# Kernel optimization log

Measured on AMD Instinct MI355X. Metric: run time of the kernel, lower is better.

Reference implementation:

```python
import jax, jax.numpy as jnp
import numpy as np

N, M, K = 100000, 50000, 8   # num vertices, num hyperedges, fixed hyperedge size
DIN, DOUT = 128, 128

def setup_inputs() -> dict:
    key = jax.random.key(0)
    k1, k2, k3 = jax.random.split(key, 3)
    X = jax.random.normal(k1, (N, DIN), jnp.float32)
    vertex = jax.random.randint(k2, (M * K,), 0, N)          # member vertices, flattened
    edges = jnp.repeat(jnp.arange(M), K)                     # hyperedge id per entry (sorted)
    W = jax.random.normal(k3, (DIN, DOUT), jnp.float32) / np.sqrt(DIN)
    b = jnp.zeros((DOUT,), jnp.float32)
    return {"X": X, "vertex": vertex, "edges": edges, "W": W, "b": b}

def reference(X, vertex, edges, W, b):
    # theta: Linear(in, out) applied BEFORE graph construction (as in dhg.HyperGCNConv)
    Y = X @ W + b                              # [N, DOUT]
    verts = vertex.reshape(M, K)               # hyperedge membership (edges = repeat(arange(M), K))
    feats = Y[verts]                           # [M, K, DOUT] gather
    # pairwise squared distances within each hyperedge
    sq = jnp.sum(feats * feats, axis=-1)                      # [M, K]
    d2 = sq[:, :, None] + sq[:, None, :] - 2.0 * jnp.einsum('mkd,mld->mkl', feats, feats)
    flat = jnp.argmax(d2.reshape(M, K * K), axis=1)
    ui, vi = flat // K, flat % K                              # argmax-distance pair positions
    u = jnp.take_along_axis(verts, ui[:, None], 1)[:, 0]      # [M]
    v = jnp.take_along_axis(verts, vi[:, None], 1)[:, 0]      # [M]
    w = jnp.float32(1.0 / (2 * K - 3))                        # HyperGCN mediator weight
    pos = jnp.arange(K)
    med = ((pos[None, :] != ui[:, None]) & (pos[None, :] != vi[:, None])).astype(Y.dtype)  # [M,K]
    # graph edges: (u,v) + (u,m),(v,m) for each mediator m; masked entries get weight 0
    src = jnp.concatenate([u, jnp.repeat(u, K), jnp.repeat(v, K)])
    dst = jnp.concatenate([v, verts.reshape(-1), verts.reshape(-1)])
    wts = jnp.concatenate([jnp.full((M,), w, Y.dtype), (med * w).reshape(-1), (med * w).reshape(-1)])
    # GCN smoothing: D^{-1/2} (A + I) D^{-1/2} Y with symmetric A, duplicate edges summed
    deg = jnp.ones((N,), Y.dtype).at[src].add(wts).at[dst].add(wts)
    dinv = jax.lax.rsqrt(deg)
    Xs = Y * dinv[:, None]
    out = Xs                                                  # self-loop term
    out = out.at[dst].add(wts[:, None] * Xs[src])
    out = out.at[src].add(wts[:, None] * Xs[dst])
    out = out * dinv[:, None]
    return jax.nn.relu(out)                                   # is_last=False -> ReLU (dropout=0)
```

## Files before the change

### kernel.cpp

```cpp
#include <hip/hip_runtime.h>
#include <hip/hip_bf16.h>

#define NV 100000
#define ME 50000
#define NINC (ME * 8)
#define NBLK ((NV + 255) / 256)
constexpr float WMED = 1.0f / 13.0f;

typedef __attribute__((ext_vector_type(8))) short bf16x8;
typedef __attribute__((ext_vector_type(4))) float f32x4;

static __device__ inline void cvt_split8(const float4& a, const float4& b,
                                         bf16x8& hi, bf16x8& lo) {
    const float v[8] = {a.x, a.y, a.z, a.w, b.x, b.y, b.z, b.w};
    #pragma unroll
    for (int j = 0; j < 8; ++j) {
        __hip_bfloat16 h = __float2bfloat16(v[j]);
        const float hf = __bfloat162float(h);
        __hip_bfloat16 l = __float2bfloat16(v[j] - hf);
        union { __hip_bfloat16 b; short s; } uh{h}, ul{l};
        hi[j] = uh.s;
        lo[j] = ul.s;
    }
}

__global__ __launch_bounds__(512, 4) void k_gemm(const float* __restrict__ X,
                                                 const float* __restrict__ W,
                                                 const float* __restrict__ bias,
                                                 float* __restrict__ Y,
                                                 __hip_bfloat16* __restrict__ Ybf) {
    __shared__ bf16x8 sWh[2048];
    __shared__ bf16x8 sWl[2048];
    const int t = threadIdx.x;
    const int wv = t >> 6;
    const int L  = t & 63;
    const int m  = L & 15;
    const int q  = L >> 4;

    for (int idx = t; idx < 128 * 32; idx += 512) {
        const int k  = idx >> 5;
        const int c4 = (idx & 31) * 4;
        const float4 w = *(const float4*)(W + (long)k * 128 + c4);
        const float wv4[4] = {w.x, w.y, w.z, w.w};
        short* swh = (short*)sWh;
        short* swl = (short*)sWl;
        const int s = k >> 5, qq = (k >> 3) & 3, j = k & 7;
        #pragma unroll
        for (int j2 = 0; j2 < 4; ++j2) {
            const int c = c4 + j2;
            const int frag = (s * 8 + (c >> 4)) * 64 + qq * 16 + (c & 15);
            __hip_bfloat16 h = __float2bfloat16(wv4[j2]);
            const float hf = __bfloat162float(h);
            __hip_bfloat16 l = __float2bfloat16(wv4[j2] - hf);
            union { __hip_bfloat16 b; short s; } uh{h}, ul{l};
            swh[frag * 8 + j] = uh.s;
            swl[frag * 8 + j] = ul.s;
        }
    }
    __syncthreads();

    f32x4 acc[2][8];
    #pragma unroll
    for (int tt = 0; tt < 2; ++tt)
        #pragma unroll
        for (int g = 0; g < 8; ++g)
            acc[tt][g] = (f32x4){0.f, 0.f, 0.f, 0.f};

    const int row_base = blockIdx.x * 256 + wv * 32;
    int r0 = row_base + m;      if (r0 > NV - 1) r0 = NV - 1;
    int r1 = row_base + 16 + m; if (r1 > NV - 1) r1 = NV - 1;

    #pragma unroll
    for (int s = 0; s < 4; ++s) {
        const int kb = s * 32 + q * 8;
        const float4 a00 = *(const float4*)(X + (long)r0 * 128 + kb);
        const float4 a01 = *(const float4*)(X + (long)r0 * 128 + kb + 4);
        const float4 a10 = *(const float4*)(X + (long)r1 * 128 + kb);
        const float4 a11 = *(const float4*)(X + (long)r1 * 128 + kb + 4);
        bf16x8 ah0, al0, ah1, al1;
        cvt_split8(a00, a01, ah0, al0);
        cvt_split8(a10, a11, ah1, al1);
        #pragma unroll
        for (int g = 0; g < 8; ++g) {
            const bf16x8 bh = sWh[(s * 8 + g) * 64 + L];
            const bf16x8 bl = sWl[(s * 8 + g) * 64 + L];
            acc[0][g] = __builtin_amdgcn_mfma_f32_16x16x32_bf16(ah0, bh, acc[0][g], 0, 0, 0);
            acc[0][g] = __builtin_amdgcn_mfma_f32_16x16x32_bf16(ah0, bl, acc[0][g], 0, 0, 0);
            acc[0][g] = __builtin_amdgcn_mfma_f32_16x16x32_bf16(al0, bh, acc[0][g], 0, 0, 0);
            acc[1][g] = __builtin_amdgcn_mfma_f32_16x16x32_bf16(ah1, bh, acc[1][g], 0, 0, 0);
            acc[1][g] = __builtin_amdgcn_mfma_f32_16x16x32_bf16(ah1, bl, acc[1][g], 0, 0, 0);
            acc[1][g] = __builtin_amdgcn_mfma_f32_16x16x32_bf16(al1, bh, acc[1][g], 0, 0, 0);
        }
    }

    #pragma unroll
    for (int g = 0; g < 8; ++g) {
        const int col = g * 16 + m;
        const float bc = bias[col];
        #pragma unroll
        for (int tt = 0; tt < 2; ++tt) {
            #pragma unroll
            for (int r = 0; r < 4; ++r) {
                const int row = row_base + tt * 16 + q * 4 + r;
                const float v = acc[tt][g][r] + bc;
                const float vn = __shfl_xor(v, 1);
                if (row < NV) {
                    Y[(long)row * 128 + col] = v;
                    if ((L & 1) == 0) {
                        __hip_bfloat162 h2;
                        h2.x = __float2bfloat16(v);
                        h2.y = __float2bfloat16(vn);
                        *(__hip_bfloat162*)(Ybf + (long)row * 128 + col) = h2;
                    }
                }
            }
        }
    }
}

__global__ __launch_bounds__(256) void k_edge(const float* __restrict__ Y,
                                              const int* __restrict__ vertex,
                                              int* __restrict__ uvpos) {
    __shared__ float sF[4][8 * 132];
    const int wid = threadIdx.x >> 6;
    const int lane = threadIdx.x & 63;
    const int m = blockIdx.x * 4 + wid;
    float* F = sF[wid];

    int verts[8];
    #pragma unroll
    for (int p = 0; p < 8; ++p) verts[p] = vertex[m * 8 + p];

    #pragma unroll
    for (int p = 0; p < 8; ++p) {
        const float2 v = *(const float2*)(Y + (long)verts[p] * 128 + lane * 2);
        *(float2*)(F + p * 132 + lane * 2) = v;
    }
    __syncthreads();

    const int k = lane >> 3, l = lane & 7;
    float acc = 0.0f;
    const float4* ra = (const float4*)(F + k * 132);
    const float4* rb = (const float4*)(F + l * 132);
    #pragma unroll
    for (int d4 = 0; d4 < 32; ++d4) {
        const float4 a = ra[d4], b = rb[d4];
        acc = fmaf(a.x, b.x, acc);
        acc = fmaf(a.y, b.y, acc);
        acc = fmaf(a.z, b.z, acc);
        acc = fmaf(a.w, b.w, acc);
    }
    const float sqk = __shfl(acc, k * 9);
    const float sql = __shfl(acc, l * 9);
    float v = sqk + sql - 2.0f * acc;
    int idx = lane;
    #pragma unroll
    for (int off = 32; off >= 1; off >>= 1) {
        const float ov = __shfl_xor(v, off);
        const int oi = __shfl_xor(idx, off);
        if (ov > v || (ov == v && oi < idx)) { v = ov; idx = oi; }
    }
    if (lane == 0) uvpos[m] = idx;
}

__global__ __launch_bounds__(256) void k_init(int* __restrict__ cnt,
                                              int* __restrict__ rowptr) {
    const int i = blockIdx.x * 256 + threadIdx.x;
    if (i < NV) cnt[i] = 0;
    if (i == 0) rowptr[NV] = NINC;
}

__global__ __launch_bounds__(256) void k_hist(const int* __restrict__ vertex,
                                              int* __restrict__ cnt) {
    const int j = blockIdx.x * 256 + threadIdx.x;
    if (j < NINC) atomicAdd(cnt + vertex[j], 1);
}

__global__ __launch_bounds__(256) void k_scan1(const int* __restrict__ cnt,
                                               int* __restrict__ bsum) {
    __shared__ int s[256];
    const int t = threadIdx.x;
    const int i = blockIdx.x * 256 + t;
    s[t] = (i < NV) ? cnt[i] : 0;
    __syncthreads();
    #pragma unroll
    for (int off = 128; off >= 1; off >>= 1) {
        if (t < off) s[t] += s[t + off];
        __syncthreads();
    }
    if (t == 0) bsum[blockIdx.x] = s[0];
}

__global__ __launch_bounds__(64) void k_scan2(const int* __restrict__ bsum,
                                              int* __restrict__ boff) {
    const int lane = threadIdx.x;
    int running = 0;
    for (int c = 0; c * 64 < NBLK; ++c) {
        const int idx = c * 64 + lane;
        int v = (idx < NBLK) ? bsum[idx] : 0;
        int x = v;
        #pragma unroll
        for (int off = 1; off < 64; off <<= 1) {
            const int n = __shfl_up(x, off);
            if (lane >= off) x += n;
        }
        if (idx < NBLK) boff[idx] = running + x - v;
        running += __shfl(x, 63);
    }
}

__global__ __launch_bounds__(256) void k_scan3(const int* __restrict__ cnt,
                                               const int* __restrict__ boff,
                                               int* __restrict__ rowptr,
                                               int* __restrict__ fill) {
    __shared__ int s[256];
    const int t = threadIdx.x;
    const int i = blockIdx.x * 256 + t;
    const int v = (i < NV) ? cnt[i] : 0;
    s[t] = v;
    __syncthreads();
    #pragma unroll
    for (int off = 1; off < 256; off <<= 1) {
        const int add = (t >= off) ? s[t - off] : 0;
        __syncthreads();
        s[t] += add;
        __syncthreads();
    }
    if (i < NV) {
        const int excl = boff[blockIdx.x] + s[t] - v;
        rowptr[i] = excl;
        fill[i] = excl;
    }
}

__global__ __launch_bounds__(256) void k_fill(const int* __restrict__ vertex,
                                              const int* __restrict__ uvpos,
                                              int* __restrict__ fill,
                                              int* __restrict__ entries) {
    const int j = blockIdx.x * 256 + threadIdx.x;
    if (j < NINC) {
        const int v = vertex[j];
        const int m = j >> 3, p = j & 7;
        const int idx = uvpos[m];
        const int role = (p == (idx >> 3) || p == (idx & 7)) ? 0 : 1;
        const int slot = atomicAdd(fill + v, 1);
        entries[slot] = (m << 1) | role;
    }
}

__global__ __launch_bounds__(256) void k_deg(const int* __restrict__ rowptr,
                                             const int* __restrict__ entries,
                                             float* __restrict__ deg) {
    const int i = blockIdx.x * 256 + threadIdx.x;
    if (i >= NV) return;
    const int start = rowptr[i], end = rowptr[i + 1];
    float d = 1.0f;
    for (int e = start; e < end; ++e)
        d += (entries[e] & 1) ? (2.0f * WMED) : (7.0f * WMED);
    deg[i] = d;
}

__global__ __launch_bounds__(256) void k_sp(const __hip_bfloat16* __restrict__ Ybf,
                                            const int* __restrict__ vertex,
                                            const int* __restrict__ uvpos,
                                            const float* __restrict__ deg,
                                            __hip_bfloat162* __restrict__ SP) {
    const int wid = threadIdx.x >> 6;
    const int lane = threadIdx.x & 63;
    const int m = blockIdx.x * 4 + wid;

    const int idx = uvpos[m];
    const int ui = idx >> 3, vi = idx & 7;

    float S0 = 0.f, S1 = 0.f, U0 = 0.f, U1 = 0.f, V0 = 0.f, V1 = 0.f;
    #pragma unroll
    for (int p = 0; p < 8; ++p) {
        const int vp = vertex[m * 8 + p];
        const float di = rsqrtf(deg[vp]);
        const __hip_bfloat162 y2 =
            ((const __hip_bfloat162*)(Ybf + (long)vp * 128))[lane];
        const float r0 = __bfloat162float(y2.x) * di;
        const float r1 = __bfloat162float(y2.y) * di;
        S0 += r0; S1 += r1;
        if (p == ui) { U0 = r0; U1 = r1; }
        if (p == vi) { V0 = r0; V1 = r1; }
    }
    __hip_bfloat162 s2, p2;
    s2.x = __float2bfloat16(WMED * S0);
    s2.y = __float2bfloat16(WMED * S1);
    p2.x = __float2bfloat16(WMED * (U0 + V0));
    p2.y = __float2bfloat16(WMED * (U1 + V1));
    SP[(long)(2 * m) * 64 + lane] = s2;
    SP[(long)(2 * m + 1) * 64 + lane] = p2;
}

__global__ __launch_bounds__(256) void k_gather(const float* __restrict__ Y,
                                                const float* __restrict__ deg,
                                                const int* __restrict__ rowptr,
                                                const int* __restrict__ entries,
                                                const __hip_bfloat162* __restrict__ SP,
                                                float* __restrict__ out) {
    const int wid = threadIdx.x >> 6;
    const int lane = threadIdx.x & 63;
    const int i = blockIdx.x * 4 + wid;

    const int start = rowptr[i], end = rowptr[i + 1];
    const int degc = end - start;
    const int tl = (lane < degc) ? entries[start + lane] : 0;

    const float din = rsqrtf(deg[i]);
    const float2 y = *(const float2*)(Y + (long)i * 128 + lane * 2);
    const float xs0 = y.x * din;
    const float xs1 = y.y * din;

    float a0 = 0.f, a1 = 0.f;
    float fnuv = 0.f;
    const int dmain = (degc < 64) ? degc : 64;

    for (int e = 0; e < dmain; e += 4) {
        const int j1 = (e + 1 < dmain) ? e + 1 : e;
        const int j2 = (e + 2 < dmain) ? e + 2 : e;
        const int j3 = (e + 3 < dmain) ? e + 3 : e;
        const float m1 = (e + 1 < dmain) ? 1.f : 0.f;
        const float m2 = (e + 2 < dmain) ? 1.f : 0.f;
        const float m3 = (e + 3 < dmain) ? 1.f : 0.f;
        const int t0 = __shfl(tl, e);
        const int t1 = __shfl(tl, j1);
        const int t2 = __shfl(tl, j2);
        const int t3 = __shfl(tl, j3);
        const __hip_bfloat162 T0 = SP[(long)t0 * 64 + lane];
        const __hip_bfloat162 T1 = SP[(long)t1 * 64 + lane];
        const __hip_bfloat162 T2 = SP[(long)t2 * 64 + lane];
        const __hip_bfloat162 T3 = SP[(long)t3 * 64 + lane];
        fnuv += (float)((t0 & 1) ^ 1) + m1 * (float)((t1 & 1) ^ 1)
              + m2 * (float)((t2 & 1) ^ 1) + m3 * (float)((t3 & 1) ^ 1);
        a0 += __bfloat162float(T0.x) + m1 * __bfloat162float(T1.x)
            + m2 * __bfloat162float(T2.x) + m3 * __bfloat162float(T3.x);
        a1 += __bfloat162float(T0.y) + m1 * __bfloat162float(T1.y)
            + m2 * __bfloat162float(T2.y) + m3 * __bfloat162float(T3.y);
    }
    for (int e2 = start + 64; e2 < end; ++e2) {
        const int t = entries[e2];
        const __hip_bfloat162 T = SP[(long)t * 64 + lane];
        fnuv += (float)((t & 1) ^ 1);
        a0 += __bfloat162float(T.x);
        a1 += __bfloat162float(T.y);
    }

    const float self = 1.0f - WMED * fnuv;
    a0 = fmaf(self, xs0, a0);
    a1 = fmaf(self, xs1, a1);
    float2 o;
    o.x = fmaxf(a0 * din, 0.0f);
    o.y = fmaxf(a1 * din, 0.0f);
    *(float2*)(out + (long)i * 128 + lane * 2) = o;
}

extern "C" void kernel_launch(void* const* d_in, const int* in_sizes, int n_in,
                              void* d_out, int out_size, void* d_ws, size_t ws_size,
                              hipStream_t stream) {
    const float* X      = (const float*)d_in[0];
    const int*   vertex = (const int*)d_in[1];
    const float* W      = (const float*)d_in[3];
    const float* bias   = (const float*)d_in[4];
    float* out = (float*)d_out;

    float* Y              = (float*)d_ws;
    __hip_bfloat16* Ybf   = (__hip_bfloat16*)(Y + (long)NV * 128);
    __hip_bfloat162* SP   = (__hip_bfloat162*)(Ybf + (long)NV * 128);
    float* deg            = (float*)((__hip_bfloat16*)SP + (long)2 * ME * 128);
    int*   uvpos          = (int*)(deg + NV);
    int*   cnt            = uvpos + ME;
    int*   rowptr         = cnt + NV;
    int*   fill           = rowptr + NV + 1;
    int*   bsum           = fill + NV;
    int*   boff           = bsum + NBLK;
    int*   entries        = boff + NBLK;

    k_gemm <<<(NV + 255) / 256, 512, 0, stream>>>(X, W, bias, Y, Ybf);
    k_edge <<<ME / 4, 256, 0, stream>>>(Y, vertex, uvpos);
    k_init <<<NBLK, 256, 0, stream>>>(cnt, rowptr);
    k_hist <<<(NINC + 255) / 256, 256, 0, stream>>>(vertex, cnt);
    k_scan1<<<NBLK, 256, 0, stream>>>(cnt, bsum);
    k_scan2<<<1, 64, 0, stream>>>(bsum, boff);
    k_scan3<<<NBLK, 256, 0, stream>>>(cnt, boff, rowptr, fill);
    k_fill <<<(NINC + 255) / 256, 256, 0, stream>>>(vertex, uvpos, fill, entries);
    k_deg  <<<NBLK, 256, 0, stream>>>(rowptr, entries, deg);
    k_sp   <<<ME / 4, 256, 0, stream>>>(Ybf, vertex, uvpos, deg, SP);
    k_gather<<<NV / 4, 256, 0, stream>>>(Y, deg, rowptr, entries, SP, out);
}
```

Before: 276.8 us.

## Precompute split-bf16 W fragments once and split GEMM across column halves

The W hi/lo bf16 split and fragment reordering move out of every GEMM block into a small pre-pass kernel that writes them to workspace. Each GEMM block now loads a pre-laid-out half of W (64 columns) straight into shared memory and computes only that column half, so the grid doubles and shared memory and accumulators per block halve. Launch bounds rise to allow more resident blocks. The cost is that each X row tile is read and split into bf16 twice (once per column half), plus one extra kernel launch.

```diff
diff --git a/kernel.cpp b/kernel.cpp
--- a/kernel.cpp
+++ b/kernel.cpp
@@ -24,49 +24,56 @@
     }
 }
 
-__global__ __launch_bounds__(512, 4) void k_gemm(const float* __restrict__ X,
-                                                 const float* __restrict__ W,
+__global__ __launch_bounds__(256) void k_wsplit(const float* __restrict__ W,
+                                                short* __restrict__ Wg) {
+    const int idx = blockIdx.x * 256 + threadIdx.x;
+    const int k = idx >> 7;
+    const int c = idx & 127;
+    const float w = W[idx];
+    __hip_bfloat16 h = __float2bfloat16(w);
+    const float hf = __bfloat162float(h);
+    __hip_bfloat16 l = __float2bfloat16(w - hf);
+    const int cb = c >> 6, gp = (c >> 4) & 3, m = c & 15;
+    const int s = k >> 5, qq = (k >> 3) & 3, j = k & 7;
+    const int base = cb * 1024 + (s * 4 + gp) * 64 + qq * 16 + m;
+    union { __hip_bfloat16 b; short s; } uh{h}, ul{l};
+    Wg[(long)base * 8 + j] = uh.s;
+    Wg[(long)(2048 + base) * 8 + j] = ul.s;
+}
+
+__global__ __launch_bounds__(512, 6) void k_gemm(const float* __restrict__ X,
+                                                 const uint4* __restrict__ Wg,
                                                  const float* __restrict__ bias,
                                                  float* __restrict__ Y,
                                                  __hip_bfloat16* __restrict__ Ybf) {
-    __shared__ bf16x8 sWh[2048];
-    __shared__ bf16x8 sWl[2048];
+    __shared__ uint4 sW[2048];
     const int t = threadIdx.x;
     const int wv = t >> 6;
     const int L  = t & 63;
     const int m  = L & 15;
     const int q  = L >> 4;
 
-    for (int idx = t; idx < 128 * 32; idx += 512) {
-        const int k  = idx >> 5;
-        const int c4 = (idx & 31) * 4;
-        const float4 w = *(const float4*)(W + (long)k * 128 + c4);
-        const float wv4[4] = {w.x, w.y, w.z, w.w};
-        short* swh = (short*)sWh;
-        short* swl = (short*)sWl;
-        const int s = k >> 5, qq = (k >> 3) & 3, j = k & 7;
-        #pragma unroll
-        for (int j2 = 0; j2 < 4; ++j2) {
-            const int c = c4 + j2;
-            const int frag = (s * 8 + (c >> 4)) * 64 + qq * 16 + (c & 15);
-            __hip_bfloat16 h = __float2bfloat16(wv4[j2]);
-            const float hf = __bfloat162float(h);
-            __hip_bfloat16 l = __float2bfloat16(wv4[j2] - hf);
-            union { __hip_bfloat16 b; short s; } uh{h}, ul{l};
-            swh[frag * 8 + j] = uh.s;
-            swl[frag * 8 + j] = ul.s;
-        }
+    const int rb = blockIdx.x >> 1;
+    const int cb = blockIdx.x & 1;
+
+    #pragma unroll
+    for (int f = 0; f < 4; ++f) {
+        const int fi = f * 512 + t;
+        const int mat = fi >> 10, loc = fi & 1023;
+        sW[fi] = Wg[(long)mat * 2048 + cb * 1024 + loc];
     }
     __syncthreads();
 
-    f32x4 acc[2][8];
+    const bf16x8* sWf = (const bf16x8*)sW;
+
+    f32x4 acc[2][4];
     #pragma unroll
     for (int tt = 0; tt < 2; ++tt)
         #pragma unroll
-        for (int g = 0; g < 8; ++g)
+        for (int g = 0; g < 4; ++g)
             acc[tt][g] = (f32x4){0.f, 0.f, 0.f, 0.f};
 
-    const int row_base = blockIdx.x * 256 + wv * 32;
+    const int row_base = rb * 256 + wv * 32;
     int r0 = row_base + m;      if (r0 > NV - 1) r0 = NV - 1;
     int r1 = row_base + 16 + m; if (r1 > NV - 1) r1 = NV - 1;
 
@@ -81,9 +88,9 @@
         cvt_split8(a00, a01, ah0, al0);
         cvt_split8(a10, a11, ah1, al1);
         #pragma unroll
-        for (int g = 0; g < 8; ++g) {
-            const bf16x8 bh = sWh[(s * 8 + g) * 64 + L];
-            const bf16x8 bl = sWl[(s * 8 + g) * 64 + L];
+        for (int g = 0; g < 4; ++g) {
+            const bf16x8 bh = sWf[(s * 4 + g) * 64 + L];
+            const bf16x8 bl = sWf[1024 + (s * 4 + g) * 64 + L];
             acc[0][g] = __builtin_amdgcn_mfma_f32_16x16x32_bf16(ah0, bh, acc[0][g], 0, 0, 0);
             acc[0][g] = __builtin_amdgcn_mfma_f32_16x16x32_bf16(ah0, bl, acc[0][g], 0, 0, 0);
             acc[0][g] = __builtin_amdgcn_mfma_f32_16x16x32_bf16(al0, bh, acc[0][g], 0, 0, 0);
@@ -94,8 +101,8 @@
     }
 
     #pragma unroll
-    for (int g = 0; g < 8; ++g) {
-        const int col = g * 16 + m;
+    for (int g = 0; g < 4; ++g) {
+        const int col = cb * 64 + g * 16 + m;
         const float bc = bias[col];
         #pragma unroll
         for (int tt = 0; tt < 2; ++tt) {
@@ -376,8 +383,11 @@
     int*   bsum           = fill + NV;
     int*   boff           = bsum + NBLK;
     int*   entries        = boff + NBLK;
-
-    k_gemm <<<(NV + 255) / 256, 512, 0, stream>>>(X, W, bias, Y, Ybf);
+    char*  pW             = (char*)(entries + NINC);
+    uint4* Wg             = (uint4*)(((uintptr_t)pW + 15) & ~(uintptr_t)15);
+
+    k_wsplit<<<64, 256, 0, stream>>>(W, (short*)Wg);
+    k_gemm <<<NBLK * 2, 512, 0, stream>>>(X, Wg, bias, Y, Ybf);
     k_edge <<<ME / 4, 256, 0, stream>>>(Y, vertex, uvpos);
     k_init <<<NBLK, 256, 0, stream>>>(cnt, rowptr);
     k_hist <<<(NINC + 255) / 256, 256, 0, stream>>>(vertex, cnt);
```

After: 272.0 us. About the same (-1.7%).
